# Performance work log

Measured on AMD Instinct MI355X. Metric: run time of the kernel, lower is better.

Reference implementation:

```python
import jax, jax.numpy as jnp
import numpy as np

BS, NR, VDIM, QDIM, CSUB, RDIM = 64, 36, 2048, 1024, 512, 256


def setup_inputs() -> dict:
    key = jax.random.key(0)
    ks = jax.random.split(key, 8)
    s = 0.02  # weight scale
    return {
        "X": jax.random.normal(ks[0], (BS, NR, VDIM), jnp.float32),
        "Q": jax.random.normal(ks[1], (BS, QDIM), jnp.float32),
        "pos": jax.random.uniform(ks[2], (BS, NR, 4), jnp.float32),
        "Wv": jax.random.normal(ks[3], (VDIM + 4, CSUB), jnp.float32) * s,
        "bv": jnp.zeros((CSUB,), jnp.float32),
        "Wq": jax.random.normal(ks[4], (QDIM, CSUB), jnp.float32) * s,
        "bq": jnp.zeros((CSUB,), jnp.float32),
        "W1": jax.random.normal(ks[5], (CSUB, RDIM), jnp.float32) * s,
        "b1": jnp.zeros((RDIM,), jnp.float32),
        "W2": jax.random.normal(ks[6], (RDIM, RDIM), jnp.float32) * s,
        "b2": jnp.zeros((RDIM,), jnp.float32),
    }


def reference(X, Q, pos, Wv, bv, Wq, bq, W1, b1, W2, b2):
    # pe_enable: concat position encodings -> [bs, Nr, v_dim+4]
    Xc = jnp.concatenate([X, pos], axis=-1)
    # FCNet projections (weight-norm linear + ReLU; dropout identity in eval)
    Xp = jax.nn.relu(Xc @ Wv + bv)              # [bs, Nr, C]
    Qp = jax.nn.relu(Q @ Wq + bq)               # [bs, C]
    Xs = Xp + Qp[:, None, :]                    # broadcast question over regions
    # pairwise elementwise product: pair[b,i,j,c] = Xs[b,j,c] * Xs[b,i,c]
    pair = Xs[:, None, :, :] * Xs[:, :, None, :]  # [bs, Nr, Nr, C]
    # 1x1 convs == per-(i,j) channel-mixing matmuls, relu (dropout identity)
    h = jax.nn.relu(jnp.einsum('bijc,cr->bijr', pair, W1) + b1)
    r_emb = jax.nn.relu(jnp.einsum('bijr,rs->bijs', h, W2) + b2)
    return r_emb  # [bs, Nr, Nr, r_dim]
```

## Files before the change

kernel.cpp:

```cpp
#include <hip/hip_runtime.h>
#include <hip/hip_bf16.h>
#include <stdint.h>

#define BSZ 64
#define NRG 36
#define VD  2048
#define QD  1024
#define CS  512
#define RD  256
#define KP  2080
#define MR  (BSZ*NRG)
#define TRI  666
#define TRIQ 768
#define NXB 2340

typedef __bf16 bf16x8 __attribute__((ext_vector_type(8)));
typedef float  f32x4  __attribute__((ext_vector_type(4)));

static __device__ __forceinline__ f32x4 mfma16(bf16x8 a, bf16x8 b, f32x4 c) {
    return __builtin_amdgcn_mfma_f32_16x16x32_bf16(a, b, c, 0, 0, 0);
}

static __device__ __forceinline__ void load_lds16(const __bf16* g, __bf16* l) {
    __builtin_amdgcn_global_load_lds(
        (const __attribute__((address_space(1))) uint32_t*)(const void*)g,
        (__attribute__((address_space(3))) uint32_t*)(void*)l,
        16, 0, 0);
}

__global__ __launch_bounds__(256) void k_prep(
    const float* __restrict__ X, const float* __restrict__ pos,
    const float* __restrict__ Wv, const float* __restrict__ W1,
    const float* __restrict__ W2,
    const float* __restrict__ Q, const float* __restrict__ Wq,
    const float* __restrict__ bq,
    __bf16* __restrict__ Xcg, __bf16* __restrict__ Wvg,
    __bf16* __restrict__ W1g, __bf16* __restrict__ W2g,
    int* __restrict__ lut, float* __restrict__ Qp)
{
    __shared__ float ld[32 * 65];
    int id = blockIdx.x;
    if (id < NXB) {
        int kt = id / 36, mb = id - kt * 36;
        int m0 = mb * 64;
        int r  = threadIdx.x >> 2;
        int kq = threadIdx.x & 3;
        int kbase = kt * 32 + kq * 8;
        float v[8];
        if (kbase + 7 < VD) {
            f32x4 a = *(const f32x4*)(X + (size_t)(m0 + r) * VD + kbase);
            f32x4 c = *(const f32x4*)(X + (size_t)(m0 + r) * VD + kbase + 4);
            v[0]=a[0]; v[1]=a[1]; v[2]=a[2]; v[3]=a[3];
            v[4]=c[0]; v[5]=c[1]; v[6]=c[2]; v[7]=c[3];
        } else {
            #pragma unroll
            for (int e = 0; e < 8; ++e) {
                int k = kbase + e;
                v[e] = (k < VD) ? X[(size_t)(m0 + r) * VD + k]
                     : (k < VD + 4 ? pos[(size_t)(m0 + r) * 4 + (k - VD)] : 0.f);
            }
        }
        #pragma unroll
        for (int e = 0; e < 8; ++e) ld[(kq * 8 + e) * 65 + r] = v[e];
        __syncthreads();
        int gl = threadIdx.x >> 6, rr = threadIdx.x & 63;
        bf16x8 o;
        #pragma unroll
        for (int e = 0; e < 8; ++e) o[e] = (__bf16)ld[(gl * 8 + e) * 65 + rr];
        *(bf16x8*)(Xcg + ((size_t)(kt * 4 + gl) * MR + m0 + rr) * 8) = o;
        return;
    }
    id -= NXB;
    if (id < 520 + 64 + 32) {
        const float* W; __bf16* Wg; int K, N, nbx;
        if (id < 520)      {          W = Wv; Wg = Wvg; K = VD + 4; N = CS; nbx = CS / 64; }
        else if (id < 584) { id -= 520; W = W1; Wg = W1g; K = CS;     N = RD; nbx = RD / 64; }
        else               { id -= 584; W = W2; Wg = W2g; K = RD;     N = RD; nbx = RD / 64; }
        int bx = id % nbx, by = id / nbx;
        int g = by * 4 + (threadIdx.x >> 6);
        int n = bx * 64 + (threadIdx.x & 63);
        bf16x8 v;
        #pragma unroll
        for (int e = 0; e < 8; ++e) {
            int k = g * 8 + e;
            v[e] = (__bf16)((k < K) ? W[(size_t)k * N + n] : 0.f);
        }
        *(bf16x8*)(Wg + ((size_t)g * N + n) * 8) = v;
        return;
    }
    id -= 616;
    if (id == 0) {
        for (int t = threadIdx.x; t < TRIQ; t += 256) {
            int tt = (t < TRI) ? t : (TRI - 1);
            int i = 0;
            while (tt >= NRG - i) { tt -= NRG - i; ++i; }
            lut[t] = (i << 8) | (i + tt);
        }
        return;
    }
    id -= 1;
    {
        int b   = id >> 3;
        int col = (id & 7) * 64 + (threadIdx.x & 63);
        int ks  = threadIdx.x >> 6;
        const float* q = Q  + (size_t)b * QD + ks * 256;
        const float* w = Wq + (size_t)(ks * 256) * CS + col;
        float a0 = 0.f, a1 = 0.f, a2 = 0.f, a3 = 0.f;
        #pragma unroll 4
        for (int k = 0; k < 256; k += 4) {
            a0 = fmaf(q[k],     w[(size_t)(k)     * CS], a0);
            a1 = fmaf(q[k + 1], w[(size_t)(k + 1) * CS], a1);
            a2 = fmaf(q[k + 2], w[(size_t)(k + 2) * CS], a2);
            a3 = fmaf(q[k + 3], w[(size_t)(k + 3) * CS], a3);
        }
        __shared__ float red[256];
        red[threadIdx.x] = a0 + a1 + a2 + a3;
        __syncthreads();
        if (ks == 0) {
            float v = red[threadIdx.x] + red[threadIdx.x + 64]
                    + red[threadIdx.x + 128] + red[threadIdx.x + 192] + bq[col];
            Qp[(size_t)b * CS + col] = fmaxf(v, 0.f);
        }
    }
}

__global__ __launch_bounds__(256) void k_g1(
    const __bf16* __restrict__ Xcg,
    const __bf16* __restrict__ Wvg,
    const float* __restrict__ bv,
    const float* __restrict__ Qp,
    __bf16* __restrict__ Xs)
{
    __shared__ __align__(16) __bf16 sA[4][4 * 64 * 8];
    __shared__ __align__(16) __bf16 sB[4][4 * 64 * 8];

    const int tid = threadIdx.x;
    const int lane = tid & 63;
    const int w = tid >> 6;
    const int wm = w & 1, wn = w >> 1;
    const int l15 = lane & 15, l4 = lane >> 4;
    const int m0 = blockIdx.x * 64;
    const int n0 = blockIdx.y * 64;
    const int sg = tid >> 6;
    const int sr = tid & 63;

    auto stage = [&](int kt, int slot) {
        load_lds16(Xcg + ((size_t)(kt * 4 + sg) * MR + m0 + sr) * 8,
                   &sA[slot][0] + (size_t)tid * 8);
        load_lds16(Wvg + ((size_t)(kt * 4 + sg) * CS + n0 + sr) * 8,
                   &sB[slot][0] + (size_t)tid * 8);
    };

    constexpr int NKT = KP / 32;
    stage(0, 0);
    stage(1, 1);

    f32x4 acc[2][2] = {};
    for (int kt = 0; kt < NKT; ++kt) {
        if (kt + 2 < NKT) stage(kt + 2, (kt + 2) & 3);
        if (kt + 2 < NKT)      asm volatile("s_waitcnt vmcnt(4)" ::: "memory");
        else if (kt + 1 < NKT) asm volatile("s_waitcnt vmcnt(2)" ::: "memory");
        else                   asm volatile("s_waitcnt vmcnt(0)" ::: "memory");
        __builtin_amdgcn_s_barrier();

        const __bf16* a_base = &sA[kt & 3][0];
        const __bf16* b_base = &sB[kt & 3][0];
        bf16x8 af[2], bf[2];
        #pragma unroll
        for (int f = 0; f < 2; ++f)
            af[f] = *(const bf16x8*)(a_base + ((size_t)l4 * 64 + wm * 32 + f * 16 + l15) * 8);
        #pragma unroll
        for (int g = 0; g < 2; ++g)
            bf[g] = *(const bf16x8*)(b_base + ((size_t)l4 * 64 + wn * 32 + g * 16 + l15) * 8);
        __builtin_amdgcn_s_setprio(1);
        #pragma unroll
        for (int f = 0; f < 2; ++f)
            #pragma unroll
            for (int g = 0; g < 2; ++g)
                acc[f][g] = mfma16(af[f], bf[g], acc[f][g]);
        __builtin_amdgcn_s_setprio(0);
    }

    #pragma unroll
    for (int f = 0; f < 2; ++f) {
        int row0 = m0 + wm * 32 + f * 16 + l4 * 4;
        #pragma unroll
        for (int g = 0; g < 2; ++g) {
            int col = n0 + wn * 32 + g * 16 + l15;
            float bb = bv[col];
            #pragma unroll
            for (int r = 0; r < 4; ++r) {
                int row = row0 + r;
                float v = fmaxf(acc[f][g][r] + bb, 0.f) + Qp[(size_t)(row / NRG) * CS + col];
                Xs[(size_t)row * CS + col] = (__bf16)v;
            }
        }
    }
}

__global__ __launch_bounds__(768, 1) void k_g23(
    const __bf16* __restrict__ Xs,
    const __bf16* __restrict__ W1g,
    const __bf16* __restrict__ W2g,
    const float* __restrict__ b1,
    const float* __restrict__ b2,
    float* __restrict__ Out,
    const int* __restrict__ lut)
{
    __shared__ __align__(16) __bf16 uni[32 * 192 * 8];
    __shared__ __align__(16) __bf16 sW[4][4 * RD * 8];

    const int tid = threadIdx.x;
    const int lane = tid & 63;
    const int w = tid >> 6;
    const int mg = w >> 1;
    const int nh = w & 1;
    const int l15 = lane & 15, l4 = lane >> 4;
    const int b = blockIdx.y;
    const int r_base = blockIdx.x * 192;
    const char* sXc = (const char*)uni;

    {
        const __bf16* src = Xs + (size_t)b * NRG * CS;
        #pragma unroll
        for (int it = 0; it < 3; ++it) {
            int id = it * 768 + tid;
            int r = id >> 6, cp = id & 63;
            bf16x8 v = *(const bf16x8*)(src + (size_t)r * CS + cp * 8);
            int ba = (r << 10) | ((cp ^ (r & 7)) << 4);
            *(bf16x8*)((char*)uni + ba) = v;
        }
    }
    const int t0 = r_base + mg * 32 + l15;
    const int ij0 = lut[t0], ij1 = lut[t0 + 16];
    const int i0 = ij0 >> 8, j0 = ij0 & 255;
    const int i1 = ij1 >> 8, j1 = ij1 & 255;

    asm volatile("s_waitcnt lgkmcnt(0)" ::: "memory");
    __builtin_amdgcn_s_barrier();

    auto stg_t = [&](int t) {
        if (tid < 256) {
            const __bf16* src = (t < 16) ? (W1g + (size_t)t * (RD * 32))
                                         : (W2g + (size_t)(t - 16) * (RD * 32));
            __bf16* dst = &sW[t & 3][0];
            #pragma unroll
            for (int it = 0; it < 4; ++it) {
                int c = tid + it * 256;
                load_lds16(src + (size_t)c * 8, dst + (size_t)c * 8);
            }
        }
    };

    stg_t(0);
    stg_t(1);

    f32x4 acc[2][8] = {};
    for (int t = 0; t < 16; ++t) {
        stg_t(t + 2);
        asm volatile("s_waitcnt vmcnt(8)" ::: "memory");
        __builtin_amdgcn_s_barrier();
        const int kc = t * 4 + l4;
        bf16x8 xi0 = *(const bf16x8*)(sXc + ((i0 << 10) | ((kc ^ (i0 & 7)) << 4)));
        bf16x8 xj0 = *(const bf16x8*)(sXc + ((j0 << 10) | ((kc ^ (j0 & 7)) << 4)));
        bf16x8 xi1 = *(const bf16x8*)(sXc + ((i1 << 10) | ((kc ^ (i1 & 7)) << 4)));
        bf16x8 xj1 = *(const bf16x8*)(sXc + ((j1 << 10) | ((kc ^ (j1 & 7)) << 4)));
        bf16x8 af0, af1;
        #pragma unroll
        for (int e = 0; e < 8; ++e) {
            af0[e] = (__bf16)((float)xi0[e] * (float)xj0[e]);
            af1[e] = (__bf16)((float)xi1[e] * (float)xj1[e]);
        }
        const __bf16* wb = &sW[t & 3][0];
        __builtin_amdgcn_s_setprio(1);
        #pragma unroll
        for (int g = 0; g < 8; ++g) {
            bf16x8 wf = *(const bf16x8*)(wb + ((size_t)l4 * RD + nh * 128 + g * 16 + l15) * 8);
            acc[0][g] = mfma16(af0, wf, acc[0][g]);
            acc[1][g] = mfma16(af1, wf, acc[1][g]);
        }
        __builtin_amdgcn_s_setprio(0);
    }

    __builtin_amdgcn_s_barrier();

    #pragma unroll
    for (int g = 0; g < 8; ++g) {
        int col = nh * 128 + g * 16 + l15;
        float bb = b1[col];
        int kc2 = col >> 3, e = col & 7;
        #pragma unroll
        for (int fm = 0; fm < 2; ++fm) {
            int row0 = mg * 32 + fm * 16 + l4 * 4;
            #pragma unroll
            for (int r = 0; r < 4; ++r) {
                float v = fmaxf(acc[fm][g][r] + bb, 0.f);
                uni[((size_t)kc2 * 192 + row0 + r) * 8 + e] = (__bf16)v;
            }
        }
    }
    asm volatile("s_waitcnt lgkmcnt(0)" ::: "memory");
    __builtin_amdgcn_s_barrier();

    f32x4 acc2[2][8] = {};
    for (int t = 16; t < 24; ++t) {
        if (t + 2 < 24) stg_t(t + 2);
        if (t + 2 < 24)      asm volatile("s_waitcnt vmcnt(8)" ::: "memory");
        else if (t + 1 < 24) asm volatile("s_waitcnt vmcnt(4)" ::: "memory");
        else                 asm volatile("s_waitcnt vmcnt(0)" ::: "memory");
        __builtin_amdgcn_s_barrier();
        const int kt = t - 16;
        bf16x8 ah0, ah1;
        {
            int row0 = mg * 32 + l15;
            ah0 = *(const bf16x8*)(uni + ((size_t)(kt * 4 + l4) * 192 + row0) * 8);
            ah1 = *(const bf16x8*)(uni + ((size_t)(kt * 4 + l4) * 192 + row0 + 16) * 8);
        }
        const __bf16* wb = &sW[t & 3][0];
        __builtin_amdgcn_s_setprio(1);
        #pragma unroll
        for (int g = 0; g < 8; ++g) {
            bf16x8 wf = *(const bf16x8*)(wb + ((size_t)l4 * RD + nh * 128 + g * 16 + l15) * 8);
            acc2[0][g] = mfma16(ah0, wf, acc2[0][g]);
            acc2[1][g] = mfma16(ah1, wf, acc2[1][g]);
        }
        __builtin_amdgcn_s_setprio(0);
    }

    float* uf = (float*)uni;
    float bias2[8];
    #pragma unroll
    for (int g = 0; g < 8; ++g) bias2[g] = b2[nh * 128 + g * 16 + l15];

    #pragma unroll
    for (int fm = 0; fm < 2; ++fm) {
        __syncthreads();
        #pragma unroll
        for (int g = 0; g < 8; ++g) {
            int col = nh * 128 + g * 16 + l15;
            #pragma unroll
            for (int r = 0; r < 4; ++r) {
                int row96 = mg * 16 + l4 * 4 + r;
                uf[(size_t)row96 * 256 + col] = fmaxf(acc2[fm][g][r] + bias2[g], 0.f);
            }
        }
        __syncthreads();
        #pragma unroll
        for (int k = 0; k < 8; ++k) {
            int row96 = w * 8 + k;
            int t = r_base + (row96 >> 4) * 32 + fm * 16 + (row96 & 15);
            if (t < TRI) {
                int ij = lut[t];
                int i = ij >> 8, j = ij & 255;
                f32x4 v = *(const f32x4*)&uf[(size_t)row96 * 256 + lane * 4];
                *(f32x4*)(Out + ((size_t)((b * NRG + i) * NRG + j)) * RD + lane * 4) = v;
                *(f32x4*)(Out + ((size_t)((b * NRG + j) * NRG + i)) * RD + lane * 4) = v;
            }
        }
    }
}

extern "C" void kernel_launch(void* const* d_in, const int* in_sizes, int n_in,
                              void* d_out, int out_size, void* d_ws, size_t ws_size,
                              hipStream_t stream) {
    const float* X   = (const float*)d_in[0];
    const float* Q   = (const float*)d_in[1];
    const float* pos = (const float*)d_in[2];
    const float* Wv  = (const float*)d_in[3];
    const float* bv  = (const float*)d_in[4];
    const float* Wq  = (const float*)d_in[5];
    const float* bq  = (const float*)d_in[6];
    const float* W1  = (const float*)d_in[7];
    const float* b1  = (const float*)d_in[8];
    const float* W2  = (const float*)d_in[9];
    const float* b2  = (const float*)d_in[10];

    char* ws = (char*)d_ws;
    size_t off = 0;
    auto alloc = [&](size_t bytes) {
        char* p = ws + off;
        off = (off + bytes + 255) & ~(size_t)255;
        return p;
    };
    __bf16* Xcg = (__bf16*)alloc((size_t)(KP/8) * MR * 8 * 2);
    __bf16* Wvg = (__bf16*)alloc((size_t)(KP/8) * CS * 8 * 2);
    __bf16* W1g = (__bf16*)alloc((size_t)(CS/8) * RD * 8 * 2);
    __bf16* W2g = (__bf16*)alloc((size_t)(RD/8) * RD * 8 * 2);
    float*  Qp  = (float*) alloc((size_t)BSZ * CS * 4);
    __bf16* Xs  = (__bf16*)alloc((size_t)MR * CS * 2);
    int*    lut = (int*)   alloc((size_t)TRIQ * 4);

    hipLaunchKernelGGL(k_prep, dim3(NXB + 616 + 1 + 512), dim3(256), 0, stream,
                       X, pos, Wv, W1, W2, Q, Wq, bq,
                       Xcg, Wvg, W1g, W2g, lut, Qp);
    hipLaunchKernelGGL(k_g1, dim3(MR/64, CS/64), dim3(256), 0, stream,
                       Xcg, Wvg, bv, Qp, Xs);
    hipLaunchKernelGGL(k_g23, dim3(4, BSZ), dim3(768), 0, stream,
                       Xs, W1g, W2g, b1, b2, (float*)d_out, (const int*)lut);
}
```

Measured before the change: 96.40 us.

## Halve k_g23 block to 384 threads with four M-fragments per wave

Shrinks the fused pair-product MLP kernel from 12 to 6 waves per block. Each wave now covers 64 pair rows (four 16-row fragments) instead of 32, so every weight fragment read from LDS feeds four MFMAs instead of two. The aim is less LDS weight traffic per MFMA and fewer waves contending at barriers. In exchange each wave holds twice as many accumulator registers, and with fewer waves there is less latency hiding for the staging and epilogue loops.

```diff
diff --git a/kernel.cpp b/kernel.cpp
--- a/kernel.cpp
+++ b/kernel.cpp
@@ -198,7 +198,7 @@
     }
 }
 
-__global__ __launch_bounds__(768, 1) void k_g23(
+__global__ __launch_bounds__(384, 1) void k_g23(
     const __bf16* __restrict__ Xs,
     const __bf16* __restrict__ W1g,
     const __bf16* __restrict__ W2g,
@@ -223,18 +223,22 @@
     {
         const __bf16* src = Xs + (size_t)b * NRG * CS;
         #pragma unroll
-        for (int it = 0; it < 3; ++it) {
-            int id = it * 768 + tid;
+        for (int it = 0; it < 6; ++it) {
+            int id = it * 384 + tid;
             int r = id >> 6, cp = id & 63;
             bf16x8 v = *(const bf16x8*)(src + (size_t)r * CS + cp * 8);
             int ba = (r << 10) | ((cp ^ (r & 7)) << 4);
             *(bf16x8*)((char*)uni + ba) = v;
         }
     }
-    const int t0 = r_base + mg * 32 + l15;
-    const int ij0 = lut[t0], ij1 = lut[t0 + 16];
-    const int i0 = ij0 >> 8, j0 = ij0 & 255;
-    const int i1 = ij1 >> 8, j1 = ij1 & 255;
+    int iR[4], jR[4];
+    #pragma unroll
+    for (int fm = 0; fm < 4; ++fm) {
+        int t = r_base + mg * 64 + fm * 16 + l15;
+        int ij = lut[t];
+        iR[fm] = ij >> 8;
+        jR[fm] = ij & 255;
+    }
 
     asm volatile("s_waitcnt lgkmcnt(0)" ::: "memory");
     __builtin_amdgcn_s_barrier();
@@ -255,29 +259,29 @@
     stg_t(0);
     stg_t(1);
 
-    f32x4 acc[2][8] = {};
+    f32x4 acc[4][8] = {};
     for (int t = 0; t < 16; ++t) {
         stg_t(t + 2);
         asm volatile("s_waitcnt vmcnt(8)" ::: "memory");
         __builtin_amdgcn_s_barrier();
         const int kc = t * 4 + l4;
-        bf16x8 xi0 = *(const bf16x8*)(sXc + ((i0 << 10) | ((kc ^ (i0 & 7)) << 4)));
-        bf16x8 xj0 = *(const bf16x8*)(sXc + ((j0 << 10) | ((kc ^ (j0 & 7)) << 4)));
-        bf16x8 xi1 = *(const bf16x8*)(sXc + ((i1 << 10) | ((kc ^ (i1 & 7)) << 4)));
-        bf16x8 xj1 = *(const bf16x8*)(sXc + ((j1 << 10) | ((kc ^ (j1 & 7)) << 4)));
-        bf16x8 af0, af1;
-        #pragma unroll
-        for (int e = 0; e < 8; ++e) {
-            af0[e] = (__bf16)((float)xi0[e] * (float)xj0[e]);
-            af1[e] = (__bf16)((float)xi1[e] * (float)xj1[e]);
+        bf16x8 af[4];
+        #pragma unroll
+        for (int fm = 0; fm < 4; ++fm) {
+            bf16x8 xi = *(const bf16x8*)(sXc + ((iR[fm] << 10) | ((kc ^ (iR[fm] & 7)) << 4)));
+            bf16x8 xj = *(const bf16x8*)(sXc + ((jR[fm] << 10) | ((kc ^ (jR[fm] & 7)) << 4)));
+            #pragma unroll
+            for (int e = 0; e < 8; ++e)
+                af[fm][e] = (__bf16)((float)xi[e] * (float)xj[e]);
         }
         const __bf16* wb = &sW[t & 3][0];
         __builtin_amdgcn_s_setprio(1);
         #pragma unroll
         for (int g = 0; g < 8; ++g) {
             bf16x8 wf = *(const bf16x8*)(wb + ((size_t)l4 * RD + nh * 128 + g * 16 + l15) * 8);
-            acc[0][g] = mfma16(af0, wf, acc[0][g]);
-            acc[1][g] = mfma16(af1, wf, acc[1][g]);
+            #pragma unroll
+            for (int fm = 0; fm < 4; ++fm)
+                acc[fm][g] = mfma16(af[fm], wf, acc[fm][g]);
         }
         __builtin_amdgcn_s_setprio(0);
     }
@@ -290,8 +294,8 @@
         float bb = b1[col];
         int kc2 = col >> 3, e = col & 7;
         #pragma unroll
-        for (int fm = 0; fm < 2; ++fm) {
-            int row0 = mg * 32 + fm * 16 + l4 * 4;
+        for (int fm = 0; fm < 4; ++fm) {
+            int row0 = mg * 64 + fm * 16 + l4 * 4;
             #pragma unroll
             for (int r = 0; r < 4; ++r) {
                 float v = fmaxf(acc[fm][g][r] + bb, 0.f);
@@ -302,7 +306,7 @@
     asm volatile("s_waitcnt lgkmcnt(0)" ::: "memory");
     __builtin_amdgcn_s_barrier();
 
-    f32x4 acc2[2][8] = {};
+    f32x4 acc2[4][8] = {};
     for (int t = 16; t < 24; ++t) {
         if (t + 2 < 24) stg_t(t + 2);
         if (t + 2 < 24)      asm volatile("s_waitcnt vmcnt(8)" ::: "memory");
@@ -310,19 +314,19 @@
         else                 asm volatile("s_waitcnt vmcnt(0)" ::: "memory");
         __builtin_amdgcn_s_barrier();
         const int kt = t - 16;
-        bf16x8 ah0, ah1;
-        {
-            int row0 = mg * 32 + l15;
-            ah0 = *(const bf16x8*)(uni + ((size_t)(kt * 4 + l4) * 192 + row0) * 8);
-            ah1 = *(const bf16x8*)(uni + ((size_t)(kt * 4 + l4) * 192 + row0 + 16) * 8);
-        }
+        bf16x8 ah[4];
+        #pragma unroll
+        for (int fm = 0; fm < 4; ++fm)
+            ah[fm] = *(const bf16x8*)(uni + ((size_t)(kt * 4 + l4) * 192
+                                             + mg * 64 + fm * 16 + l15) * 8);
         const __bf16* wb = &sW[t & 3][0];
         __builtin_amdgcn_s_setprio(1);
         #pragma unroll
         for (int g = 0; g < 8; ++g) {
             bf16x8 wf = *(const bf16x8*)(wb + ((size_t)l4 * RD + nh * 128 + g * 16 + l15) * 8);
-            acc2[0][g] = mfma16(ah0, wf, acc2[0][g]);
-            acc2[1][g] = mfma16(ah1, wf, acc2[1][g]);
+            #pragma unroll
+            for (int fm = 0; fm < 4; ++fm)
+                acc2[fm][g] = mfma16(ah[fm], wf, acc2[fm][g]);
         }
         __builtin_amdgcn_s_setprio(0);
     }
@@ -333,22 +337,27 @@
     for (int g = 0; g < 8; ++g) bias2[g] = b2[nh * 128 + g * 16 + l15];
 
     #pragma unroll
-    for (int fm = 0; fm < 2; ++fm) {
+    for (int p = 0; p < 2; ++p) {
         __syncthreads();
         #pragma unroll
-        for (int g = 0; g < 8; ++g) {
-            int col = nh * 128 + g * 16 + l15;
-            #pragma unroll
-            for (int r = 0; r < 4; ++r) {
-                int row96 = mg * 16 + l4 * 4 + r;
-                uf[(size_t)row96 * 256 + col] = fmaxf(acc2[fm][g][r] + bias2[g], 0.f);
+        for (int f16 = 0; f16 < 2; ++f16) {
+            int fm = 2 * p + f16;
+            #pragma unroll
+            for (int g = 0; g < 8; ++g) {
+                int col = nh * 128 + g * 16 + l15;
+                #pragma unroll
+                for (int r = 0; r < 4; ++r) {
+                    int row96 = mg * 32 + f16 * 16 + l4 * 4 + r;
+                    uf[(size_t)row96 * 256 + col] = fmaxf(acc2[fm][g][r] + bias2[g], 0.f);
+                }
             }
         }
         __syncthreads();
         #pragma unroll
-        for (int k = 0; k < 8; ++k) {
-            int row96 = w * 8 + k;
-            int t = r_base + (row96 >> 4) * 32 + fm * 16 + (row96 & 15);
+        for (int k = 0; k < 16; ++k) {
+            int row96 = w * 16 + k;
+            int gr = (row96 >> 5) * 64 + p * 32 + (row96 & 31);
+            int t = r_base + gr;
             if (t < TRI) {
                 int ij = lut[t];
                 int i = ij >> 8, j = ij & 255;
@@ -395,6 +404,6 @@
                        Xcg, Wvg, W1g, W2g, lut, Qp);
     hipLaunchKernelGGL(k_g1, dim3(MR/64, CS/64), dim3(256), 0, stream,
                        Xcg, Wvg, bv, Qp, Xs);
-    hipLaunchKernelGGL(k_g23, dim3(4, BSZ), dim3(768), 0, stream,
+    hipLaunchKernelGGL(k_g23, dim3(TRIQ/192, BSZ), dim3(384), 0, stream,
                        Xs, W1g, W2g, b1, b2, (float*)d_out, (const int*)lut);
 }
```

Result: slower. 100.1 us (+3.8%).
